# Optimization experiments

Measured on AMD Instinct MI355X. Metric: run time of the kernel, lower is better.

Reference implementation:

```python
import jax, jax.numpy as jnp
import numpy as np

H, W = 260, 346          # DAVIS346 sensor resolution
TEMP = 256.0             # time-decay temperature
B, T = 16, 4096          # batch, event sequence length
C = 2 * H + 2 * W        # pred channel dim = 1212


def setup_inputs() -> dict:
    key = jax.random.key(0)
    k1, k2, k3, k4, k5 = jax.random.split(key, 5)
    pred = jax.random.normal(k1, (B, T, C), dtype=jnp.float32)
    # target columns: [timestamp, y_index, x_index, polarity]
    t = jnp.sort(jax.random.uniform(k2, (B, T), minval=0.0, maxval=1.0e6), axis=1)
    y = jax.random.randint(k3, (B, T), 0, H)
    x = jax.random.randint(k4, (B, T), 0, W)
    p = jax.random.randint(k5, (B, T), 0, 2)
    target = jnp.stack([t,
                        y.astype(jnp.float32),
                        x.astype(jnp.float32),
                        p.astype(jnp.float32)], axis=-1)  # [B,T,4]
    return {"pred": pred, "target": target}


def _loss(pred, target):
    t = target[..., 0]                          # [B,T] timestamps
    y = target[..., 1].astype(jnp.int32)        # row indices
    x = target[..., 2].astype(jnp.int32)        # col indices
    p = target[..., 3]                          # polarity in {0,1}
    p_ = p[..., None]

    oh_y = jax.nn.one_hot(y, H, dtype=pred.dtype)   # [B,T,H]
    oh_x = jax.nn.one_hot(x, W, dtype=pred.dtype)   # [B,T,W]
    # scatter targets, concatenated in pred's channel layout [H0|H1|W0|W1]
    base = jnp.concatenate([oh_y * (1.0 - p_), oh_y * p_,
                            oh_x * (1.0 - p_), oh_x * p_], axis=-1)  # [B,T,C]

    # exponential time decay between consecutive events: d_i = exp(-(t_{i+1}-t_i)/TEMP)
    decay = jnp.exp(-(t[:, 1:] - t[:, :-1]) / TEMP)  # [B,T-1]

    # reverse recurrence: s_{T-1} = base_{T-1}; s_i = base_i + d_i * s_{i+1} for i = T-2..1;
    # s_0 = base_0 (torch loop stops before updating index 0)
    base_tm = jnp.swapaxes(base, 0, 1)               # [T,B,C] time-major
    decay_tm = jnp.swapaxes(decay, 0, 1)[..., None]  # [T-1,B,1]

    def step(carry, xd):
        b, d = xd
        s = b + d * carry
        return s, s

    _, ys = jax.lax.scan(step, base_tm[-1], (base_tm[:-1], decay_tm), reverse=True)
    s = jnp.concatenate([ys, base_tm[-1:]], axis=0)  # [T,B,C]
    s = s.at[0].set(base_tm[0])                      # index 0 never accumulated
    s = jnp.swapaxes(s, 0, 1)                        # [B,T,C]

    segs = [(0, H), (H, 2 * H), (2 * H, 2 * H + W), (2 * H + W, C)]
    losses = []
    for a, b in segs:
        logp = jax.nn.log_softmax(pred[..., a:b], axis=-1)
        soft = jax.nn.softmax(s[..., a:b], axis=-1)
        losses.append(-(soft * logp).sum(-1))        # soft-target CE, [B,T]
    lH0, lH1, lW0, lW1 = losses

    loss = ((lH0 + lW0) * (1.0 - p) + (lH1 + lW1) * p).mean()
    return loss


def reference(pred, target):
    return _loss(pred, target)
```

## Files before the change

kernel.cpp:

```cpp
#include <hip/hip_runtime.h>

#define HH 260
#define WW 346
#define CC 1212
#define CP 1280
#define HALF 640
#define NA 606
#define BB 16
#define TT 4096
#define INV_TEMP (1.0f/256.0f)
#define KCH 256
#define LCH 16
#define NG 16
#define GSZ 16
#define NJ 10

__global__ __launch_bounds__(64) void p1_local(const float* __restrict__ target,
                                               float* __restrict__ Lbuf) {
    const int blk = blockIdx.x;
    const int b = blk >> 8, k = blk & (KCH - 1);
    const int a = k * LCH;
    const int lane = threadIdx.x;

    __shared__ float tg[LCH][4];
    __shared__ float tnextS;
    tg[lane >> 2][lane & 3] = target[((size_t)b * TT + a) * 4 + lane];
    if (lane == 0) tnextS = (a + LCH < TT) ? target[((size_t)b * TT + a + LCH) * 4] : 0.0f;
    __syncthreads();

    float s0[NJ], s1[NJ];
#pragma unroll
    for (int j = 0; j < NJ; ++j) { s0[j] = 0.f; s1[j] = 0.f; }

    for (int li = LCH - 1; li >= 0; --li) {
        const int i = a + li;
        const float ti = tg[li][0];
        const float tn = (li == LCH - 1) ? tnextS : tg[li + 1][0];
        const float d = (i >= TT - 1) ? 0.0f : __expf(-(tn - ti) * INV_TEMP);
        const int y = (int)tg[li][1], x = (int)tg[li][2], p = (int)tg[li][3];
        const int uy = y, ux = 260 + x;
        if (p == 0) {
#pragma unroll
            for (int j = 0; j < NJ; ++j) {
                const int u = lane + 64 * j;
                const float add = (u == uy ? 1.f : 0.f) + (u == ux ? 1.f : 0.f);
                s0[j] = fmaf(s0[j], d, add);
                s1[j] *= d;
            }
        } else {
#pragma unroll
            for (int j = 0; j < NJ; ++j) {
                const int u = lane + 64 * j;
                const float add = (u == uy ? 1.f : 0.f) + (u == ux ? 1.f : 0.f);
                s1[j] = fmaf(s1[j], d, add);
                s0[j] *= d;
            }
        }
    }
    float* __restrict__ out = Lbuf + (size_t)blk * CP;
#pragma unroll
    for (int j = 0; j < NJ; ++j) {
        out[lane + 64 * j] = s0[j];
        out[HALF + lane + 64 * j] = s1[j];
    }
}

__global__ __launch_bounds__(256) void p2a(const float* __restrict__ target,
                                           const float* __restrict__ Lbuf,
                                           float* __restrict__ LCin,
                                           float* __restrict__ GroupL) {
    const int blk = blockIdx.x;
    const int ct = blk % 5;
    const int bg = blk / 5;
    const int b = bg >> 4, g = bg & 15;
    const int c = ct * 256 + threadIdx.x;

    float carry = 0.f;
#pragma unroll
    for (int kk = GSZ - 1; kk >= 0; --kk) {
        const int k = g * GSZ + kk;
        const size_t idx = ((size_t)(b * KCH + k)) * CP + c;
        LCin[idx] = carry;
        float P = 0.f;
        if (k < KCH - 1) {
            const float ta = target[((size_t)b * TT + k * LCH) * 4];
            const float te = target[((size_t)b * TT + (k + 1) * LCH) * 4];
            P = __expf(-(te - ta) * INV_TEMP);
        }
        carry = fmaf(P, carry, Lbuf[idx]);
    }
    GroupL[(size_t)bg * CP + c] = carry;
}

__global__ __launch_bounds__(256) void p2b(const float* __restrict__ target,
                                           const float* __restrict__ GroupL,
                                           float* __restrict__ SC) {
    const int blk = blockIdx.x;
    const int ct = blk % 5;
    const int b = blk / 5;
    const int c = ct * 256 + threadIdx.x;

    float carry = 0.f;
#pragma unroll
    for (int g = NG - 1; g >= 0; --g) {
        const size_t idx = ((size_t)(b * NG + g)) * CP + c;
        SC[idx] = carry;
        float GP = 0.f;
        if (g < NG - 1) {
            const float ta = target[((size_t)b * TT + g * (GSZ * LCH)) * 4];
            const float te = target[((size_t)b * TT + (g + 1) * (GSZ * LCH)) * 4];
            GP = __expf(-(te - ta) * INV_TEMP);
        }
        carry = fmaf(GP, carry, GroupL[idx]);
    }
}

__global__ __launch_bounds__(64) void p3_loss(const float* __restrict__ pred,
                                              const float* __restrict__ target,
                                              const float* __restrict__ LCin,
                                              const float* __restrict__ SC,
                                              double* __restrict__ partials) {
    const int blk = blockIdx.x;
    const int b = blk >> 8, k = blk & (KCH - 1);
    const int g = k >> 4;
    const int a = k * LCH;
    const int lane = threadIdx.x;

    __shared__ float tg[LCH][4];
    __shared__ float tnextS;
    tg[lane >> 2][lane & 3] = target[((size_t)b * TT + a) * 4 + lane];
    if (lane == 0) tnextS = (a + LCH < TT) ? target[((size_t)b * TT + a + LCH) * 4] : 0.0f;
    __syncthreads();

    float Qk = 0.f;
    if (g < NG - 1) {
        const float tge = target[((size_t)b * TT + (g + 1) * (GSZ * LCH)) * 4];
        const float tk1 = target[((size_t)b * TT + (k + 1) * LCH) * 4];
        Qk = __expf(-(tge - tk1) * INV_TEMP);
    }

    const float* __restrict__ lc = LCin + (size_t)blk * CP;
    const float* __restrict__ sc = SC + ((size_t)(b * NG + g)) * CP;
    float s0[NJ], s1[NJ];
#pragma unroll
    for (int j = 0; j < NJ; ++j) {
        const int u = lane + 64 * j;
        s0[j] = fmaf(Qk, sc[u], lc[u]);
        s1[j] = fmaf(Qk, sc[HALF + u], lc[HALF + u]);
    }

    float prA[NJ], prB[NJ];
    {
        const int p = (int)tg[LCH - 1][3];
        const float* __restrict__ prow = pred + ((size_t)b * TT + a + LCH - 1) * CC;
#pragma unroll
        for (int j = 0; j < NJ; ++j) {
            const int u = lane + 64 * j;
            const int c = (u < 260) ? p * HH + u : 2 * HH + p * WW + (u - 260);
            prA[j] = (u < NA) ? prow[c] : 0.0f;
        }
    }

    double lacc = 0.0;
    for (int li = LCH - 1; li >= 0; --li) {
        if (li > 0) {
            const int pn = (int)tg[li - 1][3];
            const float* __restrict__ prow = pred + ((size_t)b * TT + a + li - 1) * CC;
#pragma unroll
            for (int j = 0; j < NJ; ++j) {
                const int u = lane + 64 * j;
                const int c = (u < 260) ? pn * HH + u : 2 * HH + pn * WW + (u - 260);
                prB[j] = (u < NA) ? prow[c] : 0.0f;
            }
        }

        const int i = a + li;
        const float ti = tg[li][0];
        const float tn = (li == LCH - 1) ? tnextS : tg[li + 1][0];
        const float d = (i == 0 || i >= TT - 1) ? 0.0f : __expf(-(tn - ti) * INV_TEMP);
        const int y = (int)tg[li][1], x = (int)tg[li][2], p = (int)tg[li][3];
        const int uy = y, ux = 260 + x;

        float zpy = 0.f, zsy = 0.f, dty = 0.f;
        float zpx = 0.f, zsx = 0.f, dtx = 0.f;

        auto stepActive = [&](float (&SA)[NJ], float (&SO)[NJ]) {
#pragma unroll
            for (int j = 0; j < NJ; ++j) {
                const int u = lane + 64 * j;
                const float add = (u == uy ? 1.f : 0.f) + (u == ux ? 1.f : 0.f);
                SA[j] = fmaf(SA[j], d, add);
                SO[j] *= d;
                float es = __expf(SA[j]);
                float ep = __expf(prA[j]);
                if (j == NJ - 1) {
                    const float m = (u < NA) ? 1.f : 0.f;
                    es *= m; ep *= m;
                }
                if (j < 4) {
                    zpy += ep; zsy += es; dty = fmaf(es, prA[j], dty);
                } else if (j == 4) {
                    const bool isY = (u < 260);
                    zpy += isY ? ep : 0.f;
                    zsy += isY ? es : 0.f;
                    dty = fmaf(isY ? es : 0.f, prA[j], dty);
                    zpx += isY ? 0.f : ep;
                    zsx += isY ? 0.f : es;
                    dtx = fmaf(isY ? 0.f : es, prA[j], dtx);
                } else {
                    zpx += ep; zsx += es; dtx = fmaf(es, prA[j], dtx);
                }
            }
        };
        if (p == 0) stepActive(s0, s1); else stepActive(s1, s0);

#pragma unroll
        for (int off = 32; off > 0; off >>= 1) {
            zpy += __shfl_xor(zpy, off);
            zsy += __shfl_xor(zsy, off);
            dty += __shfl_xor(dty, off);
            zpx += __shfl_xor(zpx, off);
            zsx += __shfl_xor(zsx, off);
            dtx += __shfl_xor(dtx, off);
        }
        const float loss = __logf(zpy) + __logf(zpx)
                         - __fdividef(dty, zsy) - __fdividef(dtx, zsx);
        lacc += (double)loss;

#pragma unroll
        for (int j = 0; j < NJ; ++j) prA[j] = prB[j];
    }
    if (lane == 0) partials[blk] = lacc;
}

__global__ void p4_final(const double* __restrict__ partials, float* __restrict__ out) {
    const int tid = threadIdx.x;
    double sum = 0.0;
    for (int i = tid; i < BB * KCH; i += 256) sum += partials[i];
#pragma unroll
    for (int off = 32; off > 0; off >>= 1) sum += __shfl_xor(sum, off);
    __shared__ double sred[4];
    if ((tid & 63) == 0) sred[tid >> 6] = sum;
    __syncthreads();
    if (tid == 0)
        out[0] = (float)((sred[0] + sred[1] + sred[2] + sred[3]) / (double)((size_t)BB * TT));
}

extern "C" void kernel_launch(void* const* d_in, const int* in_sizes, int n_in,
                              void* d_out, int out_size, void* d_ws, size_t ws_size,
                              hipStream_t stream) {
    const float* pred   = (const float*)d_in[0];
    const float* target = (const float*)d_in[1];
    float* out = (float*)d_out;

    double* partials = (double*)d_ws;
    float* Lbuf   = (float*)((char*)d_ws + 65536);
    float* LCin   = Lbuf + (size_t)BB * KCH * CP;
    float* GroupL = LCin + (size_t)BB * KCH * CP;
    float* SC     = GroupL + (size_t)BB * NG * CP;

    p1_local<<<BB * KCH, 64, 0, stream>>>(target, Lbuf);
    p2a<<<BB * NG * 5, 256, 0, stream>>>(target, Lbuf, LCin, GroupL);
    p2b<<<BB * 5, 256, 0, stream>>>(target, GroupL, SC);
    p3_loss<<<BB * KCH, 64, 0, stream>>>(pred, target, LCin, SC, partials);
    p4_final<<<1, 256, 0, stream>>>(partials, out);
}
```

Baseline: 84.39 us.

## Fuse local chunk scan and group scan into one kernel with sparse updates

Merges the per-chunk local recurrence and the intra-group carry scan into a single kernel. Each 64-thread block walks a 256-event group over a quarter of the channels and keeps an accumulated decay factor with reciprocal-scaled sparse one-hot adds, so it no longer runs a dense fma per channel per event. This drops the Lbuf intermediate round trip and one launch. The trade-off is far fewer blocks (1024), a long serial loop per block, and the numerical risk of scaling adds by 1/D with periodic renormalisation. The group-level scan kernel also preloads its inputs and decay factors into registers before running the recurrence.

```diff
diff --git a/kernel.cpp b/kernel.cpp
--- a/kernel.cpp
+++ b/kernel.cpp
@@ -13,83 +13,84 @@
 #define LCH 16
 #define NG 16
 #define GSZ 16
+#define GLEN (GSZ * LCH)
 #define NJ 10
-
-__global__ __launch_bounds__(64) void p1_local(const float* __restrict__ target,
-                                               float* __restrict__ Lbuf) {
+#define SPLIT 4
+#define SLICE (CP / SPLIT)
+#define SREG (SLICE / 64)
+
+__global__ __launch_bounds__(64) void p12_scan(const float* __restrict__ target,
+                                               float* __restrict__ LCin,
+                                               float* __restrict__ GroupL) {
     const int blk = blockIdx.x;
-    const int b = blk >> 8, k = blk & (KCH - 1);
-    const int a = k * LCH;
+    const int sl = blk & (SPLIT - 1);
+    const int bg = blk >> 2;
+    const int b = bg >> 4, g = bg & 15;
     const int lane = threadIdx.x;
-
-    __shared__ float tg[LCH][4];
+    const int cbase = sl * SLICE;
+    const int a0 = g * GLEN;
+
+    __shared__ float tg[GLEN][4];
     __shared__ float tnextS;
-    tg[lane >> 2][lane & 3] = target[((size_t)b * TT + a) * 4 + lane];
-    if (lane == 0) tnextS = (a + LCH < TT) ? target[((size_t)b * TT + a + LCH) * 4] : 0.0f;
+    for (int idx = lane; idx < GLEN * 4; idx += 64)
+        tg[idx >> 2][idx & 3] = target[((size_t)b * TT + a0) * 4 + idx];
+    if (lane == 0) tnextS = (a0 + GLEN < TT) ? target[((size_t)b * TT + a0 + GLEN) * 4] : 0.0f;
     __syncthreads();
 
-    float s0[NJ], s1[NJ];
-#pragma unroll
-    for (int j = 0; j < NJ; ++j) { s0[j] = 0.f; s1[j] = 0.f; }
-
-    for (int li = LCH - 1; li >= 0; --li) {
-        const int i = a + li;
-        const float ti = tg[li][0];
-        const float tn = (li == LCH - 1) ? tnextS : tg[li + 1][0];
-        const float d = (i >= TT - 1) ? 0.0f : __expf(-(tn - ti) * INV_TEMP);
-        const int y = (int)tg[li][1], x = (int)tg[li][2], p = (int)tg[li][3];
-        const int uy = y, ux = 260 + x;
-        if (p == 0) {
-#pragma unroll
-            for (int j = 0; j < NJ; ++j) {
-                const int u = lane + 64 * j;
-                const float add = (u == uy ? 1.f : 0.f) + (u == ux ? 1.f : 0.f);
-                s0[j] = fmaf(s0[j], d, add);
-                s1[j] *= d;
-            }
-        } else {
-#pragma unroll
-            for (int j = 0; j < NJ; ++j) {
-                const int u = lane + 64 * j;
-                const float add = (u == uy ? 1.f : 0.f) + (u == ux ? 1.f : 0.f);
-                s1[j] = fmaf(s1[j], d, add);
-                s0[j] *= d;
-            }
-        }
-    }
-    float* __restrict__ out = Lbuf + (size_t)blk * CP;
-#pragma unroll
-    for (int j = 0; j < NJ; ++j) {
-        out[lane + 64 * j] = s0[j];
-        out[HALF + lane + 64 * j] = s1[j];
-    }
-}
-
-__global__ __launch_bounds__(256) void p2a(const float* __restrict__ target,
-                                           const float* __restrict__ Lbuf,
-                                           float* __restrict__ LCin,
-                                           float* __restrict__ GroupL) {
-    const int blk = blockIdx.x;
-    const int ct = blk % 5;
-    const int bg = blk / 5;
-    const int b = bg >> 4, g = bg & 15;
-    const int c = ct * 256 + threadIdx.x;
-
-    float carry = 0.f;
-#pragma unroll
-    for (int kk = GSZ - 1; kk >= 0; --kk) {
-        const int k = g * GSZ + kk;
-        const size_t idx = ((size_t)(b * KCH + k)) * CP + c;
-        LCin[idx] = carry;
-        float P = 0.f;
-        if (k < KCH - 1) {
-            const float ta = target[((size_t)b * TT + k * LCH) * 4];
-            const float te = target[((size_t)b * TT + (k + 1) * LCH) * 4];
-            P = __expf(-(te - ta) * INV_TEMP);
-        }
-        carry = fmaf(P, carry, Lbuf[idx]);
-    }
-    GroupL[(size_t)bg * CP + c] = carry;
+    float sig[SREG];
+#pragma unroll
+    for (int j = 0; j < SREG; ++j) sig[j] = 0.f;
+    float D = 1.f;
+
+    for (int k = GSZ - 1; k >= 0; --k) {
+        float* __restrict__ outp = LCin + ((size_t)(b * KCH + g * GSZ + k)) * CP + cbase;
+#pragma unroll
+        for (int j = 0; j < SREG; ++j) {
+            sig[j] *= D;
+            outp[lane + 64 * j] = sig[j];
+        }
+        D = 1.f;
+#pragma unroll
+        for (int q = LCH - 1; q >= 0; --q) {
+            const int li = k * LCH + q;
+            const int i = a0 + li;
+            const float ti = tg[li][0];
+            const float tn = (li == GLEN - 1) ? tnextS : tg[li + 1][0];
+            if (i < TT - 1) D *= __expf(-(tn - ti) * INV_TEMP);
+            if (D < 1e-30f) {
+#pragma unroll
+                for (int j = 0; j < SREG; ++j) sig[j] *= D;
+                D = 1.f;
+            }
+            const int y = __builtin_amdgcn_readfirstlane((int)tg[li][1]);
+            const int x = __builtin_amdgcn_readfirstlane((int)tg[li][2]);
+            const int p = __builtin_amdgcn_readfirstlane((int)tg[li][3]);
+            const float inv = __frcp_rn(D);
+            const int uy = p * HALF + y - cbase;
+            const int ux = p * HALF + 260 + x - cbase;
+            if ((unsigned)uy < (unsigned)SLICE) {
+                const float add = (lane == (uy & 63)) ? inv : 0.f;
+                const int r = uy >> 6;
+                if (r == 0) sig[0] += add;
+                else if (r == 1) sig[1] += add;
+                else if (r == 2) sig[2] += add;
+                else if (r == 3) sig[3] += add;
+                else sig[4] += add;
+            }
+            if ((unsigned)ux < (unsigned)SLICE) {
+                const float add = (lane == (ux & 63)) ? inv : 0.f;
+                const int r = ux >> 6;
+                if (r == 0) sig[0] += add;
+                else if (r == 1) sig[1] += add;
+                else if (r == 2) sig[2] += add;
+                else if (r == 3) sig[3] += add;
+                else sig[4] += add;
+            }
+        }
+    }
+    float* __restrict__ gout = GroupL + (size_t)bg * CP + cbase;
+#pragma unroll
+    for (int j = 0; j < SREG; ++j) gout[lane + 64 * j] = sig[j] * D;
 }
 
 __global__ __launch_bounds__(256) void p2b(const float* __restrict__ target,
@@ -100,18 +101,23 @@
     const int b = blk / 5;
     const int c = ct * 256 + threadIdx.x;
 
+    float Gv[NG], GP[NG];
+#pragma unroll
+    for (int g = 0; g < NG; ++g)
+        Gv[g] = GroupL[((size_t)(b * NG + g)) * CP + c];
+#pragma unroll
+    for (int g = 0; g < NG; ++g) {
+        if (g < NG - 1) {
+            const float ta = target[((size_t)b * TT + g * GLEN) * 4];
+            const float te = target[((size_t)b * TT + (g + 1) * GLEN) * 4];
+            GP[g] = __expf(-(te - ta) * INV_TEMP);
+        } else GP[g] = 0.f;
+    }
     float carry = 0.f;
 #pragma unroll
     for (int g = NG - 1; g >= 0; --g) {
-        const size_t idx = ((size_t)(b * NG + g)) * CP + c;
-        SC[idx] = carry;
-        float GP = 0.f;
-        if (g < NG - 1) {
-            const float ta = target[((size_t)b * TT + g * (GSZ * LCH)) * 4];
-            const float te = target[((size_t)b * TT + (g + 1) * (GSZ * LCH)) * 4];
-            GP = __expf(-(te - ta) * INV_TEMP);
-        }
-        carry = fmaf(GP, carry, GroupL[idx]);
+        SC[((size_t)(b * NG + g)) * CP + c] = carry;
+        carry = fmaf(GP[g], carry, Gv[g]);
     }
 }
 
@@ -134,7 +140,7 @@
 
     float Qk = 0.f;
     if (g < NG - 1) {
-        const float tge = target[((size_t)b * TT + (g + 1) * (GSZ * LCH)) * 4];
+        const float tge = target[((size_t)b * TT + (g + 1) * GLEN) * 4];
         const float tk1 = target[((size_t)b * TT + (k + 1) * LCH) * 4];
         Qk = __expf(-(tge - tk1) * INV_TEMP);
     }
@@ -254,13 +260,11 @@
     float* out = (float*)d_out;
 
     double* partials = (double*)d_ws;
-    float* Lbuf   = (float*)((char*)d_ws + 65536);
-    float* LCin   = Lbuf + (size_t)BB * KCH * CP;
+    float* LCin   = (float*)((char*)d_ws + 65536);
     float* GroupL = LCin + (size_t)BB * KCH * CP;
     float* SC     = GroupL + (size_t)BB * NG * CP;
 
-    p1_local<<<BB * KCH, 64, 0, stream>>>(target, Lbuf);
-    p2a<<<BB * NG * 5, 256, 0, stream>>>(target, Lbuf, LCin, GroupL);
+    p12_scan<<<BB * NG * SPLIT, 64, 0, stream>>>(target, LCin, GroupL);
     p2b<<<BB * 5, 256, 0, stream>>>(target, GroupL, SC);
     p3_loss<<<BB * KCH, 64, 0, stream>>>(pred, target, LCin, SC, partials);
     p4_final<<<1, 256, 0, stream>>>(partials, out);
```

After: 121.1 us. +43.5%, slower.
